# Optimization experiments

Hardware: AMD Instinct MI355X
Metric: run time of the kernel (lower is better)

The kernel has to match this reference:

```python
import jax, jax.numpy as jnp
import numpy as np

N = 100000
H = 512
E = 8
EPS = 1e-12


def _xavier(key, fan_out, fan_in):
    a = float(np.sqrt(6.0 / (fan_in + fan_out)))
    return jax.random.uniform(key, (fan_out, fan_in), jnp.float32, -a, a)


def setup_inputs() -> dict:
    key = jax.random.key(0)
    ks = jax.random.split(key, 5)
    return {
        "x": jax.random.normal(ks[0], (N, H), jnp.float32),
        "Wq": _xavier(ks[1], H, H), "bq": jnp.zeros((H,), jnp.float32),
        "Wk": _xavier(ks[2], H, H), "bk": jnp.zeros((H,), jnp.float32),
        "Wv": _xavier(ks[3], H, H), "bv": jnp.zeros((H,), jnp.float32),
        "We": _xavier(ks[4], E, H), "be": jnp.zeros((E,), jnp.float32),
    }


def reference(x, Wq, bq, Wk, bk, Wv, bv, We, be):
    n = x.shape[0]
    q = x @ Wq.T + bq                      # [N,H]
    k = x @ Wk.T + bk                      # [N,H]
    v = x @ Wv.T + bv                      # [N,H]
    q = q / jnp.maximum(jnp.linalg.norm(q), EPS)   # Frobenius norm scaling
    k = k / jnp.maximum(jnp.linalg.norm(k), EPS)
    k_sum = jnp.sum(k, axis=0)             # k^T @ ones -> [H]
    attn_norm = 1.0 + (q @ k_sum)[:, None] / n     # [N,1]
    kv = k.T @ v                           # [H,H] associative trick
    global_repr = v + (q @ kv) / n         # [N,H]
    global_repr = global_repr / jnp.maximum(attn_norm, EPS)
    global_logits = global_repr @ We.T + be        # [N,E]
    return (global_repr, global_logits)
```

## Files before the change

### kernel.cpp

```cpp
#include <hip/hip_runtime.h>
#include <hip/hip_bf16.h>
#include <stdint.h>

#define Nrows 100000
#define Hdim  512
#define Edim  8


typedef float f32x4 __attribute__((ext_vector_type(4)));
typedef short bfrag __attribute__((ext_vector_type(8)));
typedef unsigned short u16;
typedef unsigned short u16x4 __attribute__((ext_vector_type(4)));

__device__ __forceinline__ u16 f2bf(float f) {
  union { float f; uint32_t u; } v; v.f = f;
  return (u16)((v.u + 0x7FFFu + ((v.u >> 16) & 1u)) >> 16);
}
__device__ __forceinline__ float waveReduce(float p) {
  #pragma unroll
  for (int off = 32; off > 0; off >>= 1) p += __shfl_down(p, off);
  return p;
}
__device__ __forceinline__ void gload16(const u16* g, u16* l) {
  __builtin_amdgcn_global_load_lds(
      (const __attribute__((address_space(1))) void*)g,
      (__attribute__((address_space(3))) void*)l, 16, 0, 0);
}

__global__ __launch_bounds__(256) void kConv(const float* __restrict__ x, u16* __restrict__ x_bf) {
  const size_t nvec = (size_t)Nrows * Hdim / 8;
  size_t i = (size_t)blockIdx.x * 256 + threadIdx.x;
  const size_t stride = (size_t)gridDim.x * 256;
  for (size_t g = i; g < nvec; g += stride) {
    float4 v0 = ((const float4*)x)[g * 2];
    float4 v1 = ((const float4*)x)[g * 2 + 1];
    bfrag o;
    o[0] = (short)f2bf(v0.x); o[1] = (short)f2bf(v0.y);
    o[2] = (short)f2bf(v0.z); o[3] = (short)f2bf(v0.w);
    o[4] = (short)f2bf(v1.x); o[5] = (short)f2bf(v1.y);
    o[6] = (short)f2bf(v1.z); o[7] = (short)f2bf(v1.w);
    ((bfrag*)x_bf)[g] = o;
  }
}

__global__ __launch_bounds__(256) void kPrep(
    const float* __restrict__ Wv, const float* __restrict__ bv,
    const float* __restrict__ We, const float* __restrict__ be,
    u16* __restrict__ Bfin, float* __restrict__ b2e) {
  int b = blockIdx.x, t = threadIdx.x, lane = t & 63, wid = t >> 6;
  if (b < 8) {
    __shared__ float wes[512];
    for (int j = t; j < 512; j += 256) wes[j] = We[(size_t)b * Hdim + j];
    __syncthreads();
    float a0 = 0.f, a1 = 0.f;
    #pragma unroll 4
    for (int j = 0; j < 512; ++j) {
      float w = wes[j];
      a0 += w * Wv[(size_t)j * Hdim + t];
      a1 += w * Wv[(size_t)j * Hdim + t + 256];
    }
    Bfin[(size_t)(512 + b) * Hdim + t]       = f2bf(a0);
    Bfin[(size_t)(512 + b) * Hdim + t + 256] = f2bf(a1);
    if (wid == 0) {
      float p = 0.f;
      for (int j = lane; j < 512; j += 64) p += wes[j] * bv[j];
      p = waveReduce(p);
      if (lane == 0) b2e[512 + b] = p + be[b];
    }
  } else {
    int c = b - 8;
    #pragma unroll 4
    for (int i = 0; i < 32; ++i) {
      int idx = c * 32768 + i * 1024 + t * 4;
      float4 v = *(const float4*)(Wv + idx);
      u16x4 o = { f2bf(v.x), f2bf(v.y), f2bf(v.z), f2bf(v.w) };
      *(u16x4*)(Bfin + idx) = o;
    }
    if (c == 0) { b2e[t] = bv[t]; b2e[t + 256] = bv[t + 256]; }
    if (c == 1) { for (int i = t; i < 120 * 512; i += 256) Bfin[(size_t)520 * Hdim + i] = 0; }
    if (c == 2 && t < 120) b2e[520 + t] = 0.f;
  }
}

#define CPX 489
__global__ __launch_bounds__(256) void kGemm(
    const u16* __restrict__ x_bf, const u16* __restrict__ Bfin,
    const float* __restrict__ b2e, float* __restrict__ out) {
  int t5 = (blockIdx.x & 7) * CPX + (blockIdx.x >> 3);
  if (t5 >= 782 * 5) return;
  int mt = t5 / 5, nt = t5 % 5;
  int m0 = mt * 128, n0 = nt * 128;
  __shared__ u16 Alds[2][128 * 64];
  __shared__ u16 Blds[2][128 * 64];
  const int t = threadIdx.x, lane = t & 63, wid = t >> 6;
  const int wr = wid >> 1, wc = wid & 1;
  const int l15 = lane & 15, l16 = lane >> 4;

  int srcA[4], srcB[4];
  #pragma unroll
  for (int g = 0; g < 4; ++g) {
    int f = g * 256 + t;
    int row = f >> 3, slot = f & 7;
    int c = slot ^ (row & 7);
    int ar = m0 + row; if (ar > Nrows - 1) ar = Nrows - 1;
    srcA[g] = ar * Hdim + c * 8;
    srcB[g] = (n0 + row) * Hdim + c * 8;
  }
  const int ldsbase = wid * 64 * 8;

  f32x4 acc[4][4] = {};

  #pragma unroll
  for (int g = 0; g < 4; ++g) {
    gload16(x_bf + srcA[g], &Alds[0][g * 2048 + ldsbase]);
    gload16(Bfin + srcB[g], &Blds[0][g * 2048 + ldsbase]);
  }
  __syncthreads();

  for (int kt = 0; kt < 8; ++kt) {
    const int cur = kt & 1;
    if (kt < 7) {
      int k1 = (kt + 1) * 64;
      #pragma unroll
      for (int g = 0; g < 4; ++g) {
        gload16(x_bf + srcA[g] + k1, &Alds[cur ^ 1][g * 2048 + ldsbase]);
        gload16(Bfin + srcB[g] + k1, &Blds[cur ^ 1][g * 2048 + ldsbase]);
      }
    }
    #pragma unroll
    for (int ks = 0; ks < 2; ++ks) {
      bfrag af[4], bf_[4];
      #pragma unroll
      for (int mi = 0; mi < 4; ++mi) {
        int r = wr * 64 + mi * 16 + l15;
        int slot = (ks * 4 + l16) ^ (r & 7);
        af[mi] = *(const bfrag*)&Alds[cur][r * 64 + slot * 8];
      }
      #pragma unroll
      for (int ni = 0; ni < 4; ++ni) {
        int r = wc * 64 + ni * 16 + l15;
        int slot = (ks * 4 + l16) ^ (r & 7);
        bf_[ni] = *(const bfrag*)&Blds[cur][r * 64 + slot * 8];
      }
      #pragma unroll
      for (int ni = 0; ni < 4; ++ni)
        #pragma unroll
        for (int mi = 0; mi < 4; ++mi)
          acc[ni][mi] = __builtin_amdgcn_mfma_f32_16x16x32_bf16(bf_[ni], af[mi], acc[ni][mi], 0, 0, 0);
    }
    __syncthreads();
  }

  #pragma unroll
  for (int ni = 0; ni < 4; ++ni) {
    int c0 = n0 + wc * 64 + ni * 16 + l16 * 4;
    if (c0 >= 520) continue;
    f32x4 bias4 = *(const f32x4*)&b2e[c0];
    #pragma unroll
    for (int mi = 0; mi < 4; ++mi) {
      int n = m0 + wr * 64 + mi * 16 + l15;
      if (n < Nrows) {
        f32x4 v = acc[ni][mi] + bias4;
        if (c0 < Hdim)
          __builtin_nontemporal_store(v, (f32x4*)(out + (size_t)n * Hdim + c0));
        else
          __builtin_nontemporal_store(v, (f32x4*)(out + (size_t)Nrows * Hdim + (size_t)n * Edim + (c0 - Hdim)));
      }
    }
  }
}

extern "C" void kernel_launch(void* const* d_in, const int* in_sizes, int n_in,
                              void* d_out, int out_size, void* d_ws, size_t ws_size,
                              hipStream_t stream) {
  const float* x  = (const float*)d_in[0];
  const float* Wv = (const float*)d_in[5];
  const float* bv = (const float*)d_in[6];
  const float* We = (const float*)d_in[7];
  const float* be = (const float*)d_in[8];
  float* out = (float*)d_out;
  char* ws = (char*)d_ws;

  size_t off = 0;
  auto alloc = [&](size_t bytes) { size_t o = off; off += (bytes + 255) & ~(size_t)255; return o; };
  size_t o_xbf  = alloc((size_t)Nrows * Hdim * 2);
  size_t o_Bfin = alloc((size_t)640 * Hdim * 2);
  size_t o_b2e  = alloc(640 * 4);
  if (ws_size < off) return;

  u16*   x_bf = (u16*)(ws + o_xbf);
  u16*   Bfin = (u16*)(ws + o_Bfin);
  float* b2e  = (float*)(ws + o_b2e);

  kPrep<<<16,   256, 0, stream>>>(Wv, bv, We, be, Bfin, b2e);
  kConv<<<2048, 256, 0, stream>>>(x, x_bf);
  kGemm<<<8 * CPX, 256, 0, stream>>>(x_bf, Bfin, b2e, out);
}
```

Baseline: 207.2 us.

## Deepen GEMM K pipeline to four 32-wide LDS stages with explicit vmcnt waits

Splits the GEMM K-loop into 16 steps of 32 instead of 8 steps of 64. It uses a four-buffer LDS ring with loads issued two stages ahead, and waits on vmcnt counters before one barrier per step instead of a full __syncthreads drain. The LDS layout is remapped so that two rows of 32 K-elements pack into one 64-element swizzled row. The aim is to keep more global loads in flight and hide memory latency. In exchange it adds barriers per K element and depends on hand-tuned waitcnt values, which carries a correctness risk.

```diff
diff --git a/kernel.cpp b/kernel.cpp
--- a/kernel.cpp
+++ b/kernel.cpp
@@ -90,65 +90,68 @@
   if (t5 >= 782 * 5) return;
   int mt = t5 / 5, nt = t5 % 5;
   int m0 = mt * 128, n0 = nt * 128;
-  __shared__ u16 Alds[2][128 * 64];
-  __shared__ u16 Blds[2][128 * 64];
+  __shared__ u16 Alds[4][128 * 32];
+  __shared__ u16 Blds[4][128 * 32];
   const int t = threadIdx.x, lane = t & 63, wid = t >> 6;
   const int wr = wid >> 1, wc = wid & 1;
   const int l15 = lane & 15, l16 = lane >> 4;
 
-  int srcA[4], srcB[4];
-  #pragma unroll
-  for (int g = 0; g < 4; ++g) {
+  int srcA[2], srcB[2];
+  #pragma unroll
+  for (int g = 0; g < 2; ++g) {
     int f = g * 256 + t;
-    int row = f >> 3, slot = f & 7;
-    int c = slot ^ (row & 7);
-    int ar = m0 + row; if (ar > Nrows - 1) ar = Nrows - 1;
-    srcA[g] = ar * Hdim + c * 8;
-    srcB[g] = (n0 + row) * Hdim + c * 8;
-  }
-  const int ldsbase = wid * 64 * 8;
+    int R = f >> 3, s = f & 7;
+    int c8 = s ^ (R & 7);
+    int m = 2 * R + (c8 >> 2), kc = c8 & 3;
+    int ar = m0 + m; if (ar > Nrows - 1) ar = Nrows - 1;
+    srcA[g] = ar * Hdim + kc * 8;
+    srcB[g] = (n0 + m) * Hdim + kc * 8;
+  }
+  const int dst0 = wid * 512;
 
   f32x4 acc[4][4] = {};
 
   #pragma unroll
-  for (int g = 0; g < 4; ++g) {
-    gload16(x_bf + srcA[g], &Alds[0][g * 2048 + ldsbase]);
-    gload16(Bfin + srcB[g], &Blds[0][g * 2048 + ldsbase]);
-  }
-  __syncthreads();
-
-  for (int kt = 0; kt < 8; ++kt) {
-    const int cur = kt & 1;
-    if (kt < 7) {
-      int k1 = (kt + 1) * 64;
+  for (int kb = 0; kb < 2; ++kb)
+    #pragma unroll
+    for (int g = 0; g < 2; ++g) {
+      gload16(x_bf + srcA[g] + kb * 32, &Alds[kb][g * 2048 + dst0]);
+      gload16(Bfin + srcB[g] + kb * 32, &Blds[kb][g * 2048 + dst0]);
+    }
+
+  #pragma unroll
+  for (int kt = 0; kt < 16; ++kt) {
+    if (kt < 14) {
+      const int k2 = (kt + 2) * 32, b2 = (kt + 2) & 3;
       #pragma unroll
-      for (int g = 0; g < 4; ++g) {
-        gload16(x_bf + srcA[g] + k1, &Alds[cur ^ 1][g * 2048 + ldsbase]);
-        gload16(Bfin + srcB[g] + k1, &Blds[cur ^ 1][g * 2048 + ldsbase]);
+      for (int g = 0; g < 2; ++g) {
+        gload16(x_bf + srcA[g] + k2, &Alds[b2][g * 2048 + dst0]);
+        gload16(Bfin + srcB[g] + k2, &Blds[b2][g * 2048 + dst0]);
       }
     }
-    #pragma unroll
-    for (int ks = 0; ks < 2; ++ks) {
-      bfrag af[4], bf_[4];
+    if (kt < 14)       asm volatile("s_waitcnt vmcnt(8)" ::: "memory");
+    else if (kt == 14) asm volatile("s_waitcnt vmcnt(4)" ::: "memory");
+    else               asm volatile("s_waitcnt vmcnt(0)" ::: "memory");
+    __builtin_amdgcn_s_barrier();
+    const int cb = kt & 3;
+    bfrag af[4], bf_[4];
+    #pragma unroll
+    for (int mi = 0; mi < 4; ++mi) {
+      int m = wr * 64 + mi * 16 + l15, R = m >> 1;
+      int s = ((((m & 1) << 2) | l16) ^ (R & 7));
+      af[mi] = *(const bfrag*)&Alds[cb][R * 64 + s * 8];
+    }
+    #pragma unroll
+    for (int ni = 0; ni < 4; ++ni) {
+      int n_ = wc * 64 + ni * 16 + l15, R = n_ >> 1;
+      int s = ((((n_ & 1) << 2) | l16) ^ (R & 7));
+      bf_[ni] = *(const bfrag*)&Blds[cb][R * 64 + s * 8];
+    }
+    #pragma unroll
+    for (int ni = 0; ni < 4; ++ni)
       #pragma unroll
-      for (int mi = 0; mi < 4; ++mi) {
-        int r = wr * 64 + mi * 16 + l15;
-        int slot = (ks * 4 + l16) ^ (r & 7);
-        af[mi] = *(const bfrag*)&Alds[cur][r * 64 + slot * 8];
-      }
-      #pragma unroll
-      for (int ni = 0; ni < 4; ++ni) {
-        int r = wc * 64 + ni * 16 + l15;
-        int slot = (ks * 4 + l16) ^ (r & 7);
-        bf_[ni] = *(const bfrag*)&Blds[cur][r * 64 + slot * 8];
-      }
-      #pragma unroll
-      for (int ni = 0; ni < 4; ++ni)
-        #pragma unroll
-        for (int mi = 0; mi < 4; ++mi)
-          acc[ni][mi] = __builtin_amdgcn_mfma_f32_16x16x32_bf16(bf_[ni], af[mi], acc[ni][mi], 0, 0, 0);
-    }
-    __syncthreads();
+      for (int mi = 0; mi < 4; ++mi)
+        acc[ni][mi] = __builtin_amdgcn_mfma_f32_16x16x32_bf16(bf_[ni], af[mi], acc[ni][mi], 0, 0, 0);
   }
 
   #pragma unroll
```

After: 196.2 us. -5.3%, faster.

## Pre-pack B in MFMA fragment order and load it directly from global

Applied to the files above, without the earlier changes.

kPrep now writes the Wv-derived and We-fused weight matrix in a fragment-major layout that matches the 16x16x32 bf16 MFMA operand order. kGemm reads the B fragments straight from global memory (mostly L2-resident) into registers each k-step, so the B LDS buffers, their copies and their LDS reads go away. LDS per block is halved and launch bounds now ask for 3 blocks per CU to raise occupancy. The trade-off is that the B global loads are not prefetched a stage ahead, so their latency may show up inside the MFMA loop.

```diff
diff --git a/kernel.cpp b/kernel.cpp
--- a/kernel.cpp
+++ b/kernel.cpp
@@ -59,44 +59,61 @@
       a0 += w * Wv[(size_t)j * Hdim + t];
       a1 += w * Wv[(size_t)j * Hdim + t + 256];
     }
-    Bfin[(size_t)(512 + b) * Hdim + t]       = f2bf(a0);
-    Bfin[(size_t)(512 + b) * Hdim + t + 256] = f2bf(a1);
+    {
+      int kc = t >> 5, l16 = (t >> 3) & 3, e7 = t & 7;
+      Bfin[(size_t)((32 * 16 + kc) * 64 + l16 * 16 + b) * 8 + e7]       = f2bf(a0);
+      Bfin[(size_t)((32 * 16 + kc + 8) * 64 + l16 * 16 + b) * 8 + e7]   = f2bf(a1);
+    }
     if (wid == 0) {
       float p = 0.f;
       for (int j = lane; j < 512; j += 64) p += wes[j] * bv[j];
       p = waveReduce(p);
       if (lane == 0) b2e[512 + b] = p + be[b];
     }
+    bfrag z = {};
+    if (t < 64) {
+      int kc = t >> 2, l16 = t & 3;
+      *(bfrag*)(Bfin + (size_t)((32 * 16 + kc) * 64 + l16 * 16 + 8 + b) * 8) = z;
+    }
+    for (int j = t; j < 896; j += 256) {
+      int fs = 33 * 1024 + b * 896 + j;
+      *(bfrag*)(Bfin + (size_t)fs * 8) = z;
+    }
   } else {
     int c = b - 8;
     #pragma unroll 4
-    for (int i = 0; i < 32; ++i) {
-      int idx = c * 32768 + i * 1024 + t * 4;
-      float4 v = *(const float4*)(Wv + idx);
-      u16x4 o = { f2bf(v.x), f2bf(v.y), f2bf(v.z), f2bf(v.w) };
-      *(u16x4*)(Bfin + idx) = o;
+    for (int i = 0; i < 16; ++i) {
+      int u2 = c * 4096 + i * 256 + t;
+      int ng = u2 >> 10, rem = u2 & 1023;
+      int kc = rem >> 6, l16 = (rem >> 4) & 3, l15 = rem & 15;
+      const float* src = Wv + (size_t)(ng * 16 + l15) * Hdim + kc * 32 + l16 * 8;
+      float4 v0 = *(const float4*)src;
+      float4 v1 = *(const float4*)(src + 4);
+      bfrag o;
+      o[0] = (short)f2bf(v0.x); o[1] = (short)f2bf(v0.y);
+      o[2] = (short)f2bf(v0.z); o[3] = (short)f2bf(v0.w);
+      o[4] = (short)f2bf(v1.x); o[5] = (short)f2bf(v1.y);
+      o[6] = (short)f2bf(v1.z); o[7] = (short)f2bf(v1.w);
+      *(bfrag*)(Bfin + (size_t)u2 * 8) = o;
     }
     if (c == 0) { b2e[t] = bv[t]; b2e[t + 256] = bv[t + 256]; }
-    if (c == 1) { for (int i = t; i < 120 * 512; i += 256) Bfin[(size_t)520 * Hdim + i] = 0; }
-    if (c == 2 && t < 120) b2e[520 + t] = 0.f;
   }
 }
 
 #define CPX 489
-__global__ __launch_bounds__(256) void kGemm(
+__global__ __launch_bounds__(256, 3) void kGemm(
     const u16* __restrict__ x_bf, const u16* __restrict__ Bfin,
     const float* __restrict__ b2e, float* __restrict__ out) {
   int t5 = (blockIdx.x & 7) * CPX + (blockIdx.x >> 3);
   if (t5 >= 782 * 5) return;
   int mt = t5 / 5, nt = t5 % 5;
-  int m0 = mt * 128, n0 = nt * 128;
+  int m0 = mt * 128;
   __shared__ u16 Alds[2][128 * 64];
-  __shared__ u16 Blds[2][128 * 64];
   const int t = threadIdx.x, lane = t & 63, wid = t >> 6;
   const int wr = wid >> 1, wc = wid & 1;
   const int l15 = lane & 15, l16 = lane >> 4;
 
-  int srcA[4], srcB[4];
+  int srcA[4];
   #pragma unroll
   for (int g = 0; g < 4; ++g) {
     int f = g * 256 + t;
@@ -104,17 +121,15 @@
     int c = slot ^ (row & 7);
     int ar = m0 + row; if (ar > Nrows - 1) ar = Nrows - 1;
     srcA[g] = ar * Hdim + c * 8;
-    srcB[g] = (n0 + row) * Hdim + c * 8;
-  }
-  const int ldsbase = wid * 64 * 8;
+  }
+  const int dst0 = wid * 512;
+  const int ngBase = nt * 8 + wc * 4;
 
   f32x4 acc[4][4] = {};
 
   #pragma unroll
-  for (int g = 0; g < 4; ++g) {
-    gload16(x_bf + srcA[g], &Alds[0][g * 2048 + ldsbase]);
-    gload16(Bfin + srcB[g], &Blds[0][g * 2048 + ldsbase]);
-  }
+  for (int g = 0; g < 4; ++g)
+    gload16(x_bf + srcA[g], &Alds[0][g * 2048 + dst0]);
   __syncthreads();
 
   for (int kt = 0; kt < 8; ++kt) {
@@ -122,14 +137,19 @@
     if (kt < 7) {
       int k1 = (kt + 1) * 64;
       #pragma unroll
-      for (int g = 0; g < 4; ++g) {
-        gload16(x_bf + srcA[g] + k1, &Alds[cur ^ 1][g * 2048 + ldsbase]);
-        gload16(Bfin + srcB[g] + k1, &Blds[cur ^ 1][g * 2048 + ldsbase]);
-      }
-    }
+      for (int g = 0; g < 4; ++g)
+        gload16(x_bf + srcA[g] + k1, &Alds[cur ^ 1][g * 2048 + dst0]);
+    }
+    bfrag bfr[2][4];
+    #pragma unroll
+    for (int ks = 0; ks < 2; ++ks)
+      #pragma unroll
+      for (int ni = 0; ni < 4; ++ni)
+        bfr[ks][ni] = *(const bfrag*)(Bfin +
+            (size_t)((ngBase + ni) * 16 + kt * 2 + ks) * 512 + lane * 8);
     #pragma unroll
     for (int ks = 0; ks < 2; ++ks) {
-      bfrag af[4], bf_[4];
+      bfrag af[4];
       #pragma unroll
       for (int mi = 0; mi < 4; ++mi) {
         int r = wr * 64 + mi * 16 + l15;
@@ -137,23 +157,17 @@
         af[mi] = *(const bfrag*)&Alds[cur][r * 64 + slot * 8];
       }
       #pragma unroll
-      for (int ni = 0; ni < 4; ++ni) {
-        int r = wc * 64 + ni * 16 + l15;
-        int slot = (ks * 4 + l16) ^ (r & 7);
-        bf_[ni] = *(const bfrag*)&Blds[cur][r * 64 + slot * 8];
-      }
-      #pragma unroll
       for (int ni = 0; ni < 4; ++ni)
         #pragma unroll
         for (int mi = 0; mi < 4; ++mi)
-          acc[ni][mi] = __builtin_amdgcn_mfma_f32_16x16x32_bf16(bf_[ni], af[mi], acc[ni][mi], 0, 0, 0);
+          acc[ni][mi] = __builtin_amdgcn_mfma_f32_16x16x32_bf16(bfr[ks][ni], af[mi], acc[ni][mi], 0, 0, 0);
     }
     __syncthreads();
   }
 
   #pragma unroll
   for (int ni = 0; ni < 4; ++ni) {
-    int c0 = n0 + wc * 64 + ni * 16 + l16 * 4;
+    int c0 = nt * 128 + wc * 64 + ni * 16 + l16 * 4;
     if (c0 >= 520) continue;
     f32x4 bias4 = *(const f32x4*)&b2e[c0];
     #pragma unroll
@@ -184,7 +198,7 @@
   size_t off = 0;
   auto alloc = [&](size_t bytes) { size_t o = off; off += (bytes + 255) & ~(size_t)255; return o; };
   size_t o_xbf  = alloc((size_t)Nrows * Hdim * 2);
-  size_t o_Bfin = alloc((size_t)640 * Hdim * 2);
+  size_t o_Bfin = alloc((size_t)40 * 1024 * 8 * 2);
   size_t o_b2e  = alloc(640 * 4);
   if (ws_size < off) return;
 
```

After: 200.5 us. -3.2%, faster.
